# Kernel tuning notes

Measured on AMD Instinct MI355X. Metric: run time of the kernel, lower is better.

Reference implementation:

```python
import jax, jax.numpy as jnp
import numpy as np

B, T, D = 4, 8192, 1024
C = 8.0


def setup_inputs() -> dict:
    key = jax.random.key(0)
    k1, k2, k3 = jax.random.split(key, 3)
    init_std = D ** (-0.5)
    x = jax.random.normal(k1, (B, T, D), dtype=jnp.float32)
    W_in = jax.random.truncated_normal(k2, -3.0, 3.0, (D, D), dtype=jnp.float32) * init_std
    W_gate = jax.random.truncated_normal(k3, -3.0, 3.0, (D, D), dtype=jnp.float32) * init_std
    b_in = jnp.zeros((D,), dtype=jnp.float32)
    b_gate = jnp.zeros((D,), dtype=jnp.float32)
    forget_lambda = jnp.linspace(-4.323, -9.0, D, dtype=jnp.float32)
    return {"x": x, "W_in": W_in, "b_in": b_in, "W_gate": W_gate,
            "b_gate": b_gate, "forget_lambda": forget_lambda}


def _combine(c1, c2):
    # linear recurrence h_t = a_t * h_{t-1} + b_t  (associative composition)
    a1, b1 = c1
    a2, b2 = c2
    return a1 * a2, a2 * b1 + b2


def reference(x, W_in, b_in, W_gate, b_gate, forget_lambda):
    # x: [B, T, D]
    input_gate = x @ W_in.T + b_in          # [B, T, D]
    recurrence_gate = x @ W_gate.T + b_gate  # [B, T, D]
    alpha = jnp.exp(-C * jax.nn.softplus(forget_lambda) * jax.nn.sigmoid(recurrence_gate))
    beta = jnp.sqrt(1.0 - alpha ** 2 + 1e-6)
    xbeta = beta * jax.nn.sigmoid(input_gate) * x
    # parallel scan of h_t = alpha_t * h_{t-1} + xbeta_t along sequence axis
    _, h = jax.lax.associative_scan(_combine, (alpha, xbeta), axis=1)
    return h
```

## Files before the change

### kernel.cpp

```cpp
#include <hip/hip_runtime.h>

typedef unsigned short u16;
typedef __attribute__((ext_vector_type(8))) short short8;
typedef __attribute__((ext_vector_type(4))) float f32x4;

#define T_SEQ 8192
#define DDIM 1024
#define BB 4
#define MM (BB * T_SEQ)
#define NC 128
#define CHUNK (T_SEQ / NC)
#define CHAINS (BB * DDIM)

__device__ __forceinline__ float bf_lo(unsigned p) {
    union { unsigned u; float f; } v; v.u = p << 16; return v.f;
}
__device__ __forceinline__ float bf_hi(unsigned p) {
    union { unsigned u; float f; } v; v.u = p & 0xffff0000u; return v.f;
}
__device__ __forceinline__ u16 f2bf(float f) {
    union { unsigned u; float f; } v; v.f = f;
    unsigned r = v.u + 0x7fffu + ((v.u >> 16) & 1u);
    return (u16)(r >> 16);
}
__device__ __forceinline__ float sigm(float z) {
    return __builtin_amdgcn_rcpf(1.0f + __expf(-z));
}
__device__ __forceinline__ void gld16(const u16* g, u16* l) {
    __builtin_amdgcn_global_load_lds((const __attribute__((address_space(1))) void*)g,
                                     (__attribute__((address_space(3))) void*)l, 16, 0, 0);
}

__global__ __launch_bounds__(256) void cvt_bf16(const float* __restrict__ src,
                                                u16* __restrict__ dst, int n4) {
    int i = blockIdx.x * 256 + threadIdx.x;
    if (i < n4) {
        float4 v = ((const float4*)src)[i];
        ushort4 o;
        o.x = f2bf(v.x); o.y = f2bf(v.y); o.z = f2bf(v.z); o.w = f2bf(v.w);
        ((ushort4*)dst)[i] = o;
    }
}

__global__ __launch_bounds__(256, 2)
void gemm_gates(const u16* __restrict__ X, const u16* __restrict__ Wi,
                const u16* __restrict__ Wg, const float* __restrict__ b_in,
                const float* __restrict__ b_gate,
                u16* __restrict__ IG, u16* __restrict__ RG) {
    const int gate = blockIdx.z;
    const u16* __restrict__ Wp = gate ? Wg : Wi;
    const float* __restrict__ bias = gate ? b_gate : b_in;
    u16* __restrict__ outp = gate ? RG : IG;

    const int tN0 = blockIdx.x * 128;
    const int tM0 = blockIdx.y * 128;
    const int tid = threadIdx.x;
    const int lane = tid & 63;
    const int w = tid >> 6;
    const int wm = w >> 1, wn = w & 1;

    __shared__ u16 lA[128 * 32];
    __shared__ u16 lB[128 * 32];

    const u16* gA = X + (size_t)(tM0 + (tid >> 2)) * DDIM + (tid & 3) * 8;
    const u16* gB = Wp + (size_t)(tN0 + (tid >> 2)) * DDIM + (tid & 3) * 8;
    u16* lA0 = &lA[tid * 8];
    u16* lB0 = &lB[tid * 8];

    f32x4 acc[4][4] = {};

    const int lm = lane & 15;
    const int q8 = (lane >> 4) * 8;

    for (int k0 = 0; k0 < DDIM; k0 += 32) {
        __syncthreads();
        gld16(gA, lA0);
        gld16(gA + 64 * DDIM, lA0 + 2048);
        gld16(gB, lB0);
        gld16(gB + 64 * DDIM, lB0 + 2048);
        gA += 32; gB += 32;
        __syncthreads();

        short8 af[4], bfr[4];
#pragma unroll
        for (int i = 0; i < 4; i++)
            af[i] = *(const short8*)&lA[(wm * 64 + i * 16 + lm) * 32 + q8];
#pragma unroll
        for (int j = 0; j < 4; j++)
            bfr[j] = *(const short8*)&lB[(wn * 64 + j * 16 + lm) * 32 + q8];
#pragma unroll
        for (int i = 0; i < 4; i++)
#pragma unroll
            for (int j = 0; j < 4; j++)
                acc[i][j] = __builtin_amdgcn_mfma_f32_16x16x32_bf16(af[i], bfr[j], acc[i][j], 0, 0, 0);
    }

    const int r0 = (lane >> 4) << 2;
    const int cb = lane & 15;
#pragma unroll
    for (int j = 0; j < 4; j++) {
        const int colg = tN0 + wn * 64 + j * 16 + cb;
        const float bj = bias[colg];
#pragma unroll
        for (int i = 0; i < 4; i++) {
            const int rowb = tM0 + wm * 64 + i * 16 + r0;
#pragma unroll
            for (int r = 0; r < 4; r++)
                outp[(size_t)(rowb + r) * DDIM + colg] = f2bf(acc[i][j][r] + bj);
        }
    }
}

__device__ __forceinline__ void gate_eval(float nsp, float ig, float rg, float x,
                                          float& a, float& xb) {
    float sr = sigm(rg);
    a = __expf(nsp * sr);
    float be = sqrtf(1.0f - a * a + 1e-6f);
    xb = be * sigm(ig) * x;
}

__global__ __launch_bounds__(256)
void scan_pass1(const u16* __restrict__ IG, const u16* __restrict__ RG,
                const float* __restrict__ X, const float* __restrict__ lam,
                float* __restrict__ AggA, float* __restrict__ AggB) {
    const int c = blockIdx.x, dblk = blockIdx.y, b = blockIdx.z;
    const int d0 = dblk * 512 + threadIdx.x * 2;
    const float nsp0 = -8.0f * log1pf(__expf(lam[d0]));
    const float nsp1 = -8.0f * log1pf(__expf(lam[d0 + 1]));
    size_t base = ((size_t)(b * T_SEQ + c * CHUNK)) * DDIM + d0;

    float A0 = 1.0f, B0 = 0.0f, A1 = 1.0f, B1 = 0.0f;
#pragma unroll 4
    for (int t = 0; t < CHUNK; t++) {
        unsigned igp = *(const unsigned*)(IG + base);
        unsigned rgp = *(const unsigned*)(RG + base);
        float2 xv = *(const float2*)(X + base);
        float a0, xb0, a1, xb1;
        gate_eval(nsp0, bf_lo(igp), bf_lo(rgp), xv.x, a0, xb0);
        gate_eval(nsp1, bf_hi(igp), bf_hi(rgp), xv.y, a1, xb1);
        B0 = a0 * B0 + xb0; A0 *= a0;
        B1 = a1 * B1 + xb1; A1 *= a1;
        base += DDIM;
    }
    const int chain = b * DDIM + d0;
    float2 av; av.x = A0; av.y = A1;
    float2 bv; bv.x = B0; bv.y = B1;
    *(float2*)(AggA + (size_t)c * CHAINS + chain) = av;
    *(float2*)(AggB + (size_t)c * CHAINS + chain) = bv;
}

__global__ __launch_bounds__(256)
void scan_pass2(const float* __restrict__ AggA, const float* __restrict__ AggB,
                float* __restrict__ H0) {
    const int chain = blockIdx.x * 256 + threadIdx.x;
    float p = 0.0f;
    for (int c = 0; c < NC; c++) {
        H0[(size_t)c * CHAINS + chain] = p;
        p = AggA[(size_t)c * CHAINS + chain] * p + AggB[(size_t)c * CHAINS + chain];
    }
}

__global__ __launch_bounds__(256)
void scan_pass3(const u16* __restrict__ IG, const u16* __restrict__ RG,
                const float* __restrict__ X, const float* __restrict__ lam,
                const float* __restrict__ H0, float* __restrict__ out) {
    const int c = blockIdx.x, dblk = blockIdx.y, b = blockIdx.z;
    const int d0 = dblk * 512 + threadIdx.x * 2;
    const float nsp0 = -8.0f * log1pf(__expf(lam[d0]));
    const float nsp1 = -8.0f * log1pf(__expf(lam[d0 + 1]));
    size_t base = ((size_t)(b * T_SEQ + c * CHUNK)) * DDIM + d0;
    const int chain = b * DDIM + d0;

    float2 h = *(const float2*)(H0 + (size_t)c * CHAINS + chain);
#pragma unroll 4
    for (int t = 0; t < CHUNK; t++) {
        unsigned igp = *(const unsigned*)(IG + base);
        unsigned rgp = *(const unsigned*)(RG + base);
        float2 xv = *(const float2*)(X + base);
        float a0, xb0, a1, xb1;
        gate_eval(nsp0, bf_lo(igp), bf_lo(rgp), xv.x, a0, xb0);
        gate_eval(nsp1, bf_hi(igp), bf_hi(rgp), xv.y, a1, xb1);
        h.x = a0 * h.x + xb0;
        h.y = a1 * h.y + xb1;
        *(float2*)(out + base) = h;
        base += DDIM;
    }
}

extern "C" void kernel_launch(void* const* d_in, const int* in_sizes, int n_in,
                              void* d_out, int out_size, void* d_ws, size_t ws_size,
                              hipStream_t stream) {
    const float* x   = (const float*)d_in[0];
    const float* Win = (const float*)d_in[1];
    const float* bin = (const float*)d_in[2];
    const float* Wg  = (const float*)d_in[3];
    const float* bg  = (const float*)d_in[4];
    const float* lam = (const float*)d_in[5];
    float* out = (float*)d_out;

    char* w = (char*)d_ws;
    u16* Wi_bf = (u16*)(w);
    u16* Wg_bf = (u16*)(w + (size_t)(2) * 1024 * 1024);
    u16* IG    = (u16*)(w + (size_t)(4) * 1024 * 1024);
    u16* RG    = (u16*)(w + (size_t)(68) * 1024 * 1024);
    float* AggA = (float*)(w + (size_t)(132) * 1024 * 1024);
    float* AggB = (float*)(w + (size_t)(134) * 1024 * 1024);
    float* H0   = (float*)(w + (size_t)(136) * 1024 * 1024);

    u16* Xbf = (u16*)d_out;

    cvt_bf16<<<dim3((MM * DDIM / 4 + 255) / 256), dim3(256), 0, stream>>>(x, Xbf, MM * DDIM / 4);
    cvt_bf16<<<dim3((DDIM * DDIM / 4 + 255) / 256), dim3(256), 0, stream>>>(Win, Wi_bf, DDIM * DDIM / 4);
    cvt_bf16<<<dim3((DDIM * DDIM / 4 + 255) / 256), dim3(256), 0, stream>>>(Wg, Wg_bf, DDIM * DDIM / 4);

    gemm_gates<<<dim3(DDIM / 128, MM / 128, 2), dim3(256), 0, stream>>>(
        Xbf, Wi_bf, Wg_bf, bin, bg, IG, RG);

    scan_pass1<<<dim3(NC, 2, BB), dim3(256), 0, stream>>>(IG, RG, x, lam, AggA, AggB);
    scan_pass2<<<dim3(CHAINS / 256), dim3(256), 0, stream>>>(AggA, AggB, H0);
    scan_pass3<<<dim3(NC, 2, BB), dim3(256), 0, stream>>>(IG, RG, x, lam, H0, out);
}
```

Before: 544.6 us.

## Fuse both gate GEMMs sharing X tile, swizzle by XCD, vectorize scans

```diff
diff --git a/kernel.cpp b/kernel.cpp
--- a/kernel.cpp
+++ b/kernel.cpp
@@ -31,54 +31,67 @@
                                      (__attribute__((address_space(3))) void*)l, 16, 0, 0);
 }
 
-__global__ __launch_bounds__(256) void cvt_bf16(const float* __restrict__ src,
-                                                u16* __restrict__ dst, int n4) {
+#define N4X (MM * DDIM / 4)
+#define N4W (DDIM * DDIM / 4)
+__global__ __launch_bounds__(256) void cvt_all(const float* __restrict__ x,
+                                               const float* __restrict__ Wi,
+                                               const float* __restrict__ Wg,
+                                               u16* __restrict__ Xb,
+                                               u16* __restrict__ Wib,
+                                               u16* __restrict__ Wgb) {
     int i = blockIdx.x * 256 + threadIdx.x;
-    if (i < n4) {
-        float4 v = ((const float4*)src)[i];
-        ushort4 o;
-        o.x = f2bf(v.x); o.y = f2bf(v.y); o.z = f2bf(v.z); o.w = f2bf(v.w);
-        ((ushort4*)dst)[i] = o;
-    }
-}
-
-__global__ __launch_bounds__(256, 2)
-void gemm_gates(const u16* __restrict__ X, const u16* __restrict__ Wi,
+    const float* src; u16* dst; int j;
+    if (i < N4X)            { src = x;  dst = Xb;  j = i; }
+    else if (i < N4X + N4W) { src = Wi; dst = Wib; j = i - N4X; }
+    else                    { src = Wg; dst = Wgb; j = i - N4X - N4W; }
+    float4 v = ((const float4*)src)[j];
+    ushort4 o;
+    o.x = f2bf(v.x); o.y = f2bf(v.y); o.z = f2bf(v.z); o.w = f2bf(v.w);
+    ((ushort4*)dst)[j] = o;
+}
+
+__global__ __launch_bounds__(512, 4)
+void gemm_fused(const u16* __restrict__ X, const u16* __restrict__ Wi,
                 const u16* __restrict__ Wg, const float* __restrict__ b_in,
                 const float* __restrict__ b_gate,
                 u16* __restrict__ IG, u16* __restrict__ RG) {
-    const int gate = blockIdx.z;
-    const u16* __restrict__ Wp = gate ? Wg : Wi;
-    const float* __restrict__ bias = gate ? b_gate : b_in;
-    u16* __restrict__ outp = gate ? RG : IG;
-
-    const int tN0 = blockIdx.x * 128;
-    const int tM0 = blockIdx.y * 128;
+    const int b = blockIdx.x;
+    const int xcd = b & 7;
+    const int r = b >> 3;
+    const int n_tile = r & 7;
+    const int m_tile = xcd * 32 + (r >> 3);
+    const int tN0 = n_tile * 128;
+    const int tM0 = m_tile * 128;
+
     const int tid = threadIdx.x;
     const int lane = tid & 63;
     const int w = tid >> 6;
-    const int wm = w >> 1, wn = w & 1;
+    const int gate = w >> 2;
+    const int wq = w & 3;
+    const int wm = wq >> 1, wn = wq & 1;
 
     __shared__ u16 lA[128 * 32];
-    __shared__ u16 lB[128 * 32];
-
-    const u16* gA = X + (size_t)(tM0 + (tid >> 2)) * DDIM + (tid & 3) * 8;
-    const u16* gB = Wp + (size_t)(tN0 + (tid >> 2)) * DDIM + (tid & 3) * 8;
-    u16* lA0 = &lA[tid * 8];
-    u16* lB0 = &lB[tid * 8];
+    __shared__ u16 lBi[128 * 32];
+    __shared__ u16 lBg[128 * 32];
+
+    const u16* gA  = X  + (size_t)(tM0 + (tid >> 2)) * DDIM + (tid & 3) * 8;
+    const u16* gBi = Wi + (size_t)(tN0 + (tid >> 2)) * DDIM + (tid & 3) * 8;
+    const u16* gBg = Wg + (size_t)(tN0 + (tid >> 2)) * DDIM + (tid & 3) * 8;
+    u16* lA0  = &lA[tid * 8];
+    u16* lBi0 = &lBi[tid * 8];
+    u16* lBg0 = &lBg[tid * 8];
 
     f32x4 acc[4][4] = {};
-
     const int lm = lane & 15;
     const int q8 = (lane >> 4) * 8;
+    const u16* lB = gate ? lBg : lBi;
 
     for (int k0 = 0; k0 < DDIM; k0 += 32) {
         __syncthreads();
         gld16(gA, lA0);
-        gld16(gA + 64 * DDIM, lA0 + 2048);
-        gld16(gB, lB0);
-        gld16(gB + 64 * DDIM, lB0 + 2048);
-        gA += 32; gB += 32;
+        gld16(gBi, lBi0);
+        gld16(gBg, lBg0);
+        gA += 32; gBi += 32; gBg += 32;
         __syncthreads();
 
         short8 af[4], bfr[4];
@@ -95,6 +108,8 @@
                 acc[i][j] = __builtin_amdgcn_mfma_f32_16x16x32_bf16(af[i], bfr[j], acc[i][j], 0, 0, 0);
     }
 
+    u16* __restrict__ outp = gate ? RG : IG;
+    const float* __restrict__ bias = gate ? b_gate : b_in;
     const int r0 = (lane >> 4) << 2;
     const int cb = lane & 15;
 #pragma unroll
@@ -105,8 +120,8 @@
         for (int i = 0; i < 4; i++) {
             const int rowb = tM0 + wm * 64 + i * 16 + r0;
 #pragma unroll
-            for (int r = 0; r < 4; r++)
-                outp[(size_t)(rowb + r) * DDIM + colg] = f2bf(acc[i][j][r] + bj);
+            for (int rr = 0; rr < 4; rr++)
+                outp[(size_t)(rowb + rr) * DDIM + colg] = f2bf(acc[i][j][rr] + bj);
         }
     }
 }
@@ -123,30 +138,37 @@
 void scan_pass1(const u16* __restrict__ IG, const u16* __restrict__ RG,
                 const float* __restrict__ X, const float* __restrict__ lam,
                 float* __restrict__ AggA, float* __restrict__ AggB) {
-    const int c = blockIdx.x, dblk = blockIdx.y, b = blockIdx.z;
-    const int d0 = dblk * 512 + threadIdx.x * 2;
-    const float nsp0 = -8.0f * log1pf(__expf(lam[d0]));
-    const float nsp1 = -8.0f * log1pf(__expf(lam[d0 + 1]));
-    size_t base = ((size_t)(b * T_SEQ + c * CHUNK)) * DDIM + d0;
-
-    float A0 = 1.0f, B0 = 0.0f, A1 = 1.0f, B1 = 0.0f;
+    const int c = blockIdx.x, bq = blockIdx.y;
+    const int d0 = threadIdx.x * 4;
+    float nsp[4];
+#pragma unroll
+    for (int e = 0; e < 4; e++) nsp[e] = -8.0f * log1pf(__expf(lam[d0 + e]));
+    size_t base = ((size_t)(bq * T_SEQ + c * CHUNK)) * DDIM + d0;
+
+    float A[4] = {1.f, 1.f, 1.f, 1.f};
+    float Bv[4] = {0.f, 0.f, 0.f, 0.f};
 #pragma unroll 4
     for (int t = 0; t < CHUNK; t++) {
-        unsigned igp = *(const unsigned*)(IG + base);
-        unsigned rgp = *(const unsigned*)(RG + base);
-        float2 xv = *(const float2*)(X + base);
-        float a0, xb0, a1, xb1;
-        gate_eval(nsp0, bf_lo(igp), bf_lo(rgp), xv.x, a0, xb0);
-        gate_eval(nsp1, bf_hi(igp), bf_hi(rgp), xv.y, a1, xb1);
-        B0 = a0 * B0 + xb0; A0 *= a0;
-        B1 = a1 * B1 + xb1; A1 *= a1;
+        uint2 igp = *(const uint2*)(IG + base);
+        uint2 rgp = *(const uint2*)(RG + base);
+        float4 xv = *(const float4*)(X + base);
+        float igf[4] = {bf_lo(igp.x), bf_hi(igp.x), bf_lo(igp.y), bf_hi(igp.y)};
+        float rgf[4] = {bf_lo(rgp.x), bf_hi(rgp.x), bf_lo(rgp.y), bf_hi(rgp.y)};
+        float xf[4] = {xv.x, xv.y, xv.z, xv.w};
+#pragma unroll
+        for (int e = 0; e < 4; e++) {
+            float a, xb;
+            gate_eval(nsp[e], igf[e], rgf[e], xf[e], a, xb);
+            Bv[e] = a * Bv[e] + xb;
+            A[e] *= a;
+        }
         base += DDIM;
     }
-    const int chain = b * DDIM + d0;
-    float2 av; av.x = A0; av.y = A1;
-    float2 bv; bv.x = B0; bv.y = B1;
-    *(float2*)(AggA + (size_t)c * CHAINS + chain) = av;
-    *(float2*)(AggB + (size_t)c * CHAINS + chain) = bv;
+    const int chain = bq * DDIM + d0;
+    float4 av; av.x = A[0]; av.y = A[1]; av.z = A[2]; av.w = A[3];
+    float4 bv; bv.x = Bv[0]; bv.y = Bv[1]; bv.z = Bv[2]; bv.w = Bv[3];
+    *(float4*)(AggA + (size_t)c * CHAINS + chain) = av;
+    *(float4*)(AggB + (size_t)c * CHAINS + chain) = bv;
 }
 
 __global__ __launch_bounds__(256)
@@ -154,6 +176,7 @@
                 float* __restrict__ H0) {
     const int chain = blockIdx.x * 256 + threadIdx.x;
     float p = 0.0f;
+#pragma unroll 8
     for (int c = 0; c < NC; c++) {
         H0[(size_t)c * CHAINS + chain] = p;
         p = AggA[(size_t)c * CHAINS + chain] * p + AggB[(size_t)c * CHAINS + chain];
@@ -164,25 +187,32 @@
 void scan_pass3(const u16* __restrict__ IG, const u16* __restrict__ RG,
                 const float* __restrict__ X, const float* __restrict__ lam,
                 const float* __restrict__ H0, float* __restrict__ out) {
-    const int c = blockIdx.x, dblk = blockIdx.y, b = blockIdx.z;
-    const int d0 = dblk * 512 + threadIdx.x * 2;
-    const float nsp0 = -8.0f * log1pf(__expf(lam[d0]));
-    const float nsp1 = -8.0f * log1pf(__expf(lam[d0 + 1]));
-    size_t base = ((size_t)(b * T_SEQ + c * CHUNK)) * DDIM + d0;
-    const int chain = b * DDIM + d0;
-
-    float2 h = *(const float2*)(H0 + (size_t)c * CHAINS + chain);
+    const int c = blockIdx.x, bq = blockIdx.y;
+    const int d0 = threadIdx.x * 4;
+    float nsp[4];
+#pragma unroll
+    for (int e = 0; e < 4; e++) nsp[e] = -8.0f * log1pf(__expf(lam[d0 + e]));
+    size_t base = ((size_t)(bq * T_SEQ + c * CHUNK)) * DDIM + d0;
+    const int chain = bq * DDIM + d0;
+
+    float4 h = *(const float4*)(H0 + (size_t)c * CHAINS + chain);
+    float hf[4] = {h.x, h.y, h.z, h.w};
 #pragma unroll 4
     for (int t = 0; t < CHUNK; t++) {
-        unsigned igp = *(const unsigned*)(IG + base);
-        unsigned rgp = *(const unsigned*)(RG + base);
-        float2 xv = *(const float2*)(X + base);
-        float a0, xb0, a1, xb1;
-        gate_eval(nsp0, bf_lo(igp), bf_lo(rgp), xv.x, a0, xb0);
-        gate_eval(nsp1, bf_hi(igp), bf_hi(rgp), xv.y, a1, xb1);
-        h.x = a0 * h.x + xb0;
-        h.y = a1 * h.y + xb1;
-        *(float2*)(out + base) = h;
+        uint2 igp = *(const uint2*)(IG + base);
+        uint2 rgp = *(const uint2*)(RG + base);
+        float4 xv = *(const float4*)(X + base);
+        float igf[4] = {bf_lo(igp.x), bf_hi(igp.x), bf_lo(igp.y), bf_hi(igp.y)};
+        float rgf[4] = {bf_lo(rgp.x), bf_hi(rgp.x), bf_lo(rgp.y), bf_hi(rgp.y)};
+        float xf[4] = {xv.x, xv.y, xv.z, xv.w};
+#pragma unroll
+        for (int e = 0; e < 4; e++) {
+            float a, xb;
+            gate_eval(nsp[e], igf[e], rgf[e], xf[e], a, xb);
+            hf[e] = a * hf[e] + xb;
+        }
+        float4 ho; ho.x = hf[0]; ho.y = hf[1]; ho.z = hf[2]; ho.w = hf[3];
+        *(float4*)(out + base) = ho;
         base += DDIM;
     }
 }
@@ -199,24 +229,23 @@
     float* out = (float*)d_out;
 
     char* w = (char*)d_ws;
-    u16* Wi_bf = (u16*)(w);
-    u16* Wg_bf = (u16*)(w + (size_t)(2) * 1024 * 1024);
-    u16* IG    = (u16*)(w + (size_t)(4) * 1024 * 1024);
-    u16* RG    = (u16*)(w + (size_t)(68) * 1024 * 1024);
+    u16* Wi_bf  = (u16*)(w);
+    u16* Wg_bf  = (u16*)(w + (size_t)(2) * 1024 * 1024);
+    u16* IG     = (u16*)(w + (size_t)(4) * 1024 * 1024);
+    u16* RG     = (u16*)(w + (size_t)(68) * 1024 * 1024);
     float* AggA = (float*)(w + (size_t)(132) * 1024 * 1024);
     float* AggB = (float*)(w + (size_t)(134) * 1024 * 1024);
     float* H0   = (float*)(w + (size_t)(136) * 1024 * 1024);
 
     u16* Xbf = (u16*)d_out;
 
-    cvt_bf16<<<dim3((MM * DDIM / 4 + 255) / 256), dim3(256), 0, stream>>>(x, Xbf, MM * DDIM / 4);
-    cvt_bf16<<<dim3((DDIM * DDIM / 4 + 255) / 256), dim3(256), 0, stream>>>(Win, Wi_bf, DDIM * DDIM / 4);
-    cvt_bf16<<<dim3((DDIM * DDIM / 4 + 255) / 256), dim3(256), 0, stream>>>(Wg, Wg_bf, DDIM * DDIM / 4);
-
-    gemm_gates<<<dim3(DDIM / 128, MM / 128, 2), dim3(256), 0, stream>>>(
+    cvt_all<<<dim3((N4X + 2 * N4W) / 256), dim3(256), 0, stream>>>(
+        x, Win, Wg, Xbf, Wi_bf, Wg_bf);
+
+    gemm_fused<<<dim3((DDIM / 128) * (MM / 128)), dim3(512), 0, stream>>>(
         Xbf, Wi_bf, Wg_bf, bin, bg, IG, RG);
 
-    scan_pass1<<<dim3(NC, 2, BB), dim3(256), 0, stream>>>(IG, RG, x, lam, AggA, AggB);
+    scan_pass1<<<dim3(NC, BB), dim3(256), 0, stream>>>(IG, RG, x, lam, AggA, AggB);
     scan_pass2<<<dim3(CHAINS / 256), dim3(256), 0, stream>>>(AggA, AggB, H0);
-    scan_pass3<<<dim3(NC, 2, BB), dim3(256), 0, stream>>>(IG, RG, x, lam, H0, out);
-}
+    scan_pass3<<<dim3(NC, BB), dim3(256), 0, stream>>>(IG, RG, x, lam, H0, out);
+}
```

Measured after the change: 601.0 us. 1.1x slower.
